# Kernel optimization log

Measured on AMD Instinct MI355X. Metric: run time of the kernel, lower is better.

Reference implementation:

```python
import jax, jax.numpy as jnp
import numpy as np

K_NN = 3
EPS = 1e-8
MASK_THRESH = 0.5


def _three_nn_interpolate(pts, known, feats):
    """pts: (B,N,3), known: (B,M,3), feats: (B,M,C) -> (B,N,C).
    Squared-distance 3-NN + inverse-distance weighted interpolation
    (pointnet2 three_nn / three_interpolate semantics)."""
    # (B,N,M) squared euclidean distances
    d2 = (jnp.sum(pts * pts, -1)[:, :, None]
          + jnp.sum(known * known, -1)[:, None, :]
          - 2.0 * jnp.einsum('bnd,bmd->bnm', pts, known))
    neg_d, idx = jax.lax.top_k(-d2, K_NN)          # (B,N,3)
    dist = jnp.maximum(-neg_d, 0.0)                # squared dists, clamp fp error
    dist_recip = 1.0 / (dist + EPS)
    weight = dist_recip / jnp.sum(dist_recip, -1, keepdims=True)  # (B,N,3)
    b_idx = jnp.arange(pts.shape[0])[:, None, None]
    gathered = feats[b_idx, idx]                   # (B,N,3,C)
    return jnp.sum(weight[..., None] * gathered, axis=2)  # (B,N,C)


def setup_inputs() -> dict:
    key = jax.random.key(0)
    ks = jax.random.split(key, 10)
    B, N, C = 4, 8192, 32
    M2, M3, M4, Mm = 8192, 4096, 2048, 4096
    sc = 10.0  # spread coords over a realistic metric range
    return {
        'points_mean': jax.random.normal(ks[0], (B, N, 3)) * sc,
        'known2': jax.random.normal(ks[1], (B, M2, 3)) * sc,
        'feats2': jax.random.normal(ks[2], (B, M2, C)),
        'known3': jax.random.normal(ks[3], (B, M3, 3)) * sc,
        'feats3': jax.random.normal(ks[4], (B, M3, C)),
        'known4': jax.random.normal(ks[5], (B, M4, 3)) * sc,
        'feats4': jax.random.normal(ks[6], (B, M4, C)),
        'match_points': jax.random.normal(ks[7], (B, Mm, 3)) * sc,
        'w_fc': jax.random.normal(ks[8], (64, 96)) * 0.1,
        'w_cls': jax.random.normal(ks[9], (1, 64)) * 0.1,
    }


def reference(points_mean, known2, feats2, known3, feats3, known4, feats4,
              match_points, w_fc, w_cls):
    p0 = _three_nn_interpolate(points_mean, known2, feats2)  # (B,N,32)
    p1 = _three_nn_interpolate(points_mean, known3, feats3)
    p2 = _three_nn_interpolate(points_mean, known4, feats4)
    pointwise = jnp.concatenate([p0, p1, p2], axis=-1) @ w_fc.T  # (B,N,64)
    pred_hm = pointwise @ w_cls.T                                 # (B,N,1)
    # GT mask: min distance to match points < 0.5 m
    d2 = (jnp.sum(points_mean * points_mean, -1)[:, :, None]
          + jnp.sum(match_points * match_points, -1)[:, None, :]
          - 2.0 * jnp.einsum('bnd,bmd->bnm', points_mean, match_points))
    min_d = jnp.sqrt(jnp.maximum(jnp.min(d2, axis=-1), 0.0))      # (B,N)
    gt_hm = (min_d < MASK_THRESH).astype(jnp.float32)
    return pred_hm, gt_hm
```

## Files before the change

kernel.cpp:

```cpp
#include <hip/hip_runtime.h>

typedef unsigned int u32;
typedef unsigned long long u64;
typedef float f32x2 __attribute__((ext_vector_type(2)));

#define NB 4
#define NQ 8192
#define MARGIN 0.0625f
#define NBKT 4096

#define OFF_C0   0u
#define OFF_C1   (512u*1024u)
#define OFF_C2   (768u*1024u)
#define OFF_CM   (896u*1024u)
#define OFF_OI0  (1408u*1024u)
#define OFF_OI1  (1536u*1024u)
#define OFF_OI2  (1600u*1024u)
#define OFF_QSX  (1632u*1024u)
#define OFF_QSY  (1760u*1024u)
#define OFF_QSZ  (1888u*1024u)
#define OFF_QSI  (2016u*1024u)
#define OFF_BOX  (2144u*1024u)
#define WS_NEW   (2144u*1024u + 1152u*32u)
#define WS_OLD   (512u*1024 + 256u*1024 + 128u*1024 + 512u*1024)

struct __align__(32) CP { f32x2 x, y, z, w; };
struct DM { double x, y, z, w; };

__device__ __forceinline__ f32x2 fma2(f32x2 a, f32x2 b, f32x2 c) {
  return __builtin_elementwise_fma(a, b, c);
}

__device__ __forceinline__ void lexins(double& e0d, double& e1d, double& e2d,
                                       int& e0i, int& e1i, int& e2i,
                                       double d, int i) {
  if (d < e2d || (d == e2d && i < e2i)) {
    if (d < e0d || (d == e0d && i < e0i)) {
      e2d = e1d; e2i = e1i; e1d = e0d; e1i = e0i; e0d = d; e0i = i;
    } else if (d < e1d || (d == e1d && i < e1i)) {
      e2d = e1d; e2i = e1i; e1d = d; e1i = i;
    } else {
      e2d = d; e2i = i;
    }
  }
}

__device__ __forceinline__ void ins4(float kv, u32 idx,
                                     float& k0, float& k1, float& k2, float& k3,
                                     u32& i0, u32& i1, u32& i2, u32& i3) {
  if (kv < k3) {
    bool lt0 = kv < k0, lt1 = kv < k1, lt2 = kv < k2;
    k3 = lt2 ? k2 : kv;               i3 = lt2 ? i2 : idx;
    k2 = lt2 ? (lt1 ? k1 : kv) : k2;  i2 = lt2 ? (lt1 ? i1 : idx) : i2;
    k1 = lt1 ? (lt0 ? k0 : kv) : k1;  i1 = lt1 ? (lt0 ? i0 : idx) : i1;
    k0 = lt0 ? kv : k0;               i0 = lt0 ? idx : i0;
  }
}

__device__ __forceinline__ u32 spread10(u32 v) {
  v &= 0x3FFu;
  v = (v | (v << 16)) & 0x030000FFu;
  v = (v | (v << 8))  & 0x0300F00Fu;
  v = (v | (v << 4))  & 0x030C30C3u;
  v = (v | (v << 2))  & 0x09249249u;
  return v;
}
__device__ __forceinline__ u32 morton30(float x, float y, float z) {
  int xi = (int)((x + 64.f) * 8.f);
  int yi = (int)((y + 64.f) * 8.f);
  int zi = (int)((z + 64.f) * 8.f);
  xi = min(max(xi, 0), 1023); yi = min(max(yi, 0), 1023); zi = min(max(zi, 0), 1023);
  return spread10((u32)xi) | (spread10((u32)yi) << 1) | (spread10((u32)zi) << 2);
}

__global__ __launch_bounds__(512) void prep_sort(
    const float* __restrict__ k2p, const float* __restrict__ k3p,
    const float* __restrict__ k4p, const float* __restrict__ mmp,
    const float* __restrict__ pts,
    CP* __restrict__ c0, CP* __restrict__ c1, CP* __restrict__ c2,
    DM* __restrict__ cm,
    u32* __restrict__ oi0, u32* __restrict__ oi1, u32* __restrict__ oi2,
    float* __restrict__ qsx, float* __restrict__ qsy, float* __restrict__ qsz,
    u32* __restrict__ qsi, float* __restrict__ boxes) {
  __shared__ u32 ord[8192];
  __shared__ u32 hist[NBKT];
  const int arr = blockIdx.x, b = blockIdx.y, tid = threadIdx.x;
  const float* src = (arr == 0) ? k2p : (arr == 1) ? k3p : (arr == 2) ? k4p
                      : (arr == 3) ? mmp : pts;
  const int n = (arr == 0) ? 8192 : (arr == 1) ? 4096 : (arr == 2) ? 2048
                 : (arr == 3) ? 4096 : 8192;
  const float* sb = src + (size_t)b * n * 3;

  for (int i = tid; i < NBKT; i += 512) hist[i] = 0;
  __syncthreads();
  for (int i = tid; i < n; i += 512) {
    u32 bkt = morton30(sb[3 * i], sb[3 * i + 1], sb[3 * i + 2]) >> 18;
    atomicAdd(&hist[bkt], 1u);
  }
  __syncthreads();
  for (int d = 1; d < NBKT; d <<= 1) {
    for (int i = tid; i < NBKT / (2 * d); i += 512) {
      int idx = (2 * i + 2) * d - 1;
      hist[idx] += hist[idx - d];
    }
    __syncthreads();
  }
  if (tid == 0) hist[NBKT - 1] = 0;
  __syncthreads();
  for (int d = NBKT >> 1; d >= 1; d >>= 1) {
    for (int i = tid; i < NBKT / (2 * d); i += 512) {
      int idx = (2 * i + 2) * d - 1;
      u32 t = hist[idx - d];
      hist[idx - d] = hist[idx];
      hist[idx] += t;
    }
    __syncthreads();
  }
  for (int i = tid; i < n; i += 512) {
    u32 bkt = morton30(sb[3 * i], sb[3 * i + 1], sb[3 * i + 2]) >> 18;
    u32 pos = atomicAdd(&hist[bkt], 1u);
    ord[pos] = (u32)i;
  }
  __syncthreads();

  if (arr < 3) {
    CP* dst = ((arr == 0) ? c0 : (arr == 1) ? c1 : c2) + (size_t)b * (n >> 1);
    u32* oi = ((arr == 0) ? oi0 : (arr == 1) ? oi1 : oi2) + (size_t)b * n;
    for (int i = tid; i < (n >> 1); i += 512) {
      u32 p0 = ord[2 * i], p1 = ord[2 * i + 1];
      const float* a0 = sb + 3 * (size_t)p0;
      const float* a1 = sb + 3 * (size_t)p1;
      float x0 = a0[0], y0 = a0[1], z0 = a0[2];
      float x1 = a1[0], y1 = a1[1], z1 = a1[2];
      CP c;
      c.x = f32x2{x0, x1}; c.y = f32x2{y0, y1}; c.z = f32x2{z0, z1};
      c.w = f32x2{fmaf(z0, z0, fmaf(y0, y0, x0 * x0)),
                  fmaf(z1, z1, fmaf(y1, y1, x1 * x1))};
      dst[i] = c; oi[2 * i] = p0; oi[2 * i + 1] = p1;
    }
  } else if (arr == 3) {
    DM* dst = cm + (size_t)b * 4096;
    for (int i = tid; i < 4096; i += 512) {
      u32 p = ord[i];
      double x = (double)sb[3 * p], y = (double)sb[3 * p + 1], z = (double)sb[3 * p + 2];
      DM d = {x, y, z, fma(z, z, fma(y, y, x * x))};
      dst[i] = d;
    }
  } else {
    for (int i = tid; i < 8192; i += 512) {
      u32 p = ord[i];
      size_t o = (size_t)b * 8192 + i;
      qsx[o] = sb[3 * p]; qsy[o] = sb[3 * p + 1]; qsz[o] = sb[3 * p + 2];
      qsi[o] = p;
    }
  }
  if (arr < 4) {
    const int nG = n >> 6;
    const int boff = (arr == 0) ? 0 : (arr == 1) ? 512 : (arr == 2) ? 768 : 896;
    for (int g = tid; g < nG; g += 512) {
      float xlo = 1e30f, xhi = -1e30f, ylo = 1e30f, yhi = -1e30f, zlo = 1e30f, zhi = -1e30f;
      for (int j = 0; j < 64; ++j) {
        u32 p = ord[g * 64 + j];
        float x = sb[3 * p], y = sb[3 * p + 1], z = sb[3 * p + 2];
        xlo = fminf(xlo, x); xhi = fmaxf(xhi, x);
        ylo = fminf(ylo, y); yhi = fmaxf(yhi, y);
        zlo = fminf(zlo, z); zhi = fmaxf(zhi, z);
      }
      float* bx = boxes + (size_t)(boff + b * nG + g) * 8;
      bx[0] = xlo; bx[1] = xhi; bx[2] = ylo; bx[3] = yhi; bx[4] = zlo; bx[5] = zhi;
      bx[6] = 0.f; bx[7] = 0.f;
    }
  }
}

struct Smem2 {
  float  qx[64], qy[64], qz[64];
  double qdx[64], qdy[64], qdz[64], qn[64];
  u32    oq[64];
  u32    di[3][64][4][4];
  double mmin[64][8];
  float  wv[96];
  float  wq[64][9];
  u32    iq[64][9];
  float  contrib[64][9];
};

__global__ __launch_bounds__(512, 2) void fused_sorted(
    const float* __restrict__ f2, const float* __restrict__ f3,
    const float* __restrict__ f4,
    const float* __restrict__ wfc, const float* __restrict__ wcls,
    const CP* __restrict__ c0, const CP* __restrict__ c1,
    const CP* __restrict__ c2, const DM* __restrict__ cm,
    const u32* __restrict__ oi0, const u32* __restrict__ oi1,
    const u32* __restrict__ oi2,
    const float* __restrict__ qsx, const float* __restrict__ qsy,
    const float* __restrict__ qsz, const u32* __restrict__ qsi,
    const float* __restrict__ boxes, float* __restrict__ out) {
  __shared__ Smem2 s;
  const int tid = threadIdx.x;
  const int b = blockIdx.y;
  const int tile = blockIdx.x;
  const int q0 = tile * 64;
  const int qloc = tid & 63;
  const int wid = __builtin_amdgcn_readfirstlane(tid >> 6);

  if (tid < 64) {
    size_t o = (size_t)b * NQ + q0 + tid;
    float x = qsx[o], y = qsy[o], z = qsz[o];
    s.qx[tid] = x; s.qy[tid] = y; s.qz[tid] = z; s.oq[tid] = qsi[o];
    double dx = (double)x, dy = (double)y, dz = (double)z;
    s.qdx[tid] = dx; s.qdy[tid] = dy; s.qdz[tid] = dz;
    s.qn[tid] = (dx * dx + dy * dy) + dz * dz;
  } else if (tid < 160) {
    int t = tid - 64;
    float acc = 0.f;
    for (int j = 0; j < 64; ++j) acc += wcls[j] * wfc[j * 96 + t];
    s.wv[t] = acc;
  }
  __syncthreads();

  const float qx = s.qx[qloc], qy = s.qy[qloc], qz = s.qz[qloc];
  const float qnf = fmaf(qz, qz, fmaf(qy, qy, qx * qx));
  const float fm2x = -2.0f * qx, fm2y = -2.0f * qy, fm2z = -2.0f * qz;
  const double dm2x = -2.0 * s.qdx[qloc];
  const double dm2y = -2.0 * s.qdy[qloc];
  const double dm2z = -2.0 * s.qdz[qloc];

  {
    int lvl, prt, P;
    if (wid < 4)      { lvl = 0; prt = wid;     P = 4; }
    else if (wid < 6) { lvl = 1; prt = wid - 4; P = 2; }
    else              { lvl = 2; prt = wid - 6; P = 2; }
    const int M  = (lvl == 0) ? 8192 : ((lvl == 1) ? 4096 : 2048);
    const int nG = M >> 6;
    const CP* c4 = ((lvl == 0) ? c0 : ((lvl == 1) ? c1 : c2)) + (((size_t)b * M) >> 1);
    const float* bxb = boxes +
        (size_t)(((lvl == 0) ? 0 : ((lvl == 1) ? 512 : 768)) + b * nG) * 8;
    int g0 = (tile * nG) >> 7;
    g0 = (g0 & ~(P - 1)) + prt;

    float k0 = __builtin_inff(), k1 = k0, k2 = k0, k3 = k0;
    u32 i0 = 0, i1 = 0, i2 = 0, i3 = 0;
    const f32x2 mx2 = {fm2x, fm2x}, my2 = {fm2y, fm2y}, mz2 = {fm2z, fm2z};

    for (int t = 0; t < nG / P; ++t) {
      int g = (g0 + P * t) & (nG - 1);
      const float* bx = bxb + g * 8;
      float dx = fmaxf(fmaxf(bx[0] - qx, qx - bx[1]), 0.f);
      float dy = fmaxf(fmaxf(bx[2] - qy, qy - bx[3]), 0.f);
      float dz = fmaxf(fmaxf(bx[4] - qz, qz - bx[5]), 0.f);
      float lb = fmaf(dx, dx, fmaf(dy, dy, dz * dz));
      if (__any(lb < qnf + k3 + MARGIN)) {
        const CP* cg = c4 + g * 32;
#pragma unroll 2
        for (int gg = 0; gg < 32; gg += 4) {
          f32x2 key[4];
#pragma unroll
          for (int u = 0; u < 4; ++u) {
            CP c = cg[gg + u];
            key[u] = fma2(mx2, c.x, fma2(my2, c.y, fma2(mz2, c.z, c.w)));
          }
#pragma unroll
          for (int u = 0; u < 4; ++u) {
            float ka = key[u].x, kb = key[u].y;
            if (fminf(ka, kb) < k3) {
              u32 ib = (u32)((g * 32 + gg + u) * 2);
              ins4(ka, ib,     k0, k1, k2, k3, i0, i1, i2, i3);
              ins4(kb, ib + 1, k0, k1, k2, k3, i0, i1, i2, i3);
            }
          }
        }
      }
    }
    s.di[lvl][qloc][prt][0] = i0; s.di[lvl][qloc][prt][1] = i1;
    s.di[lvl][qloc][prt][2] = i2; s.di[lvl][qloc][prt][3] = i3;
  }

  {
    const DM* cmb = cm + (size_t)b * 4096;
    const float* bxb = boxes + (size_t)(896 + b * 64) * 8;
    int gm0 = ((tile * 64) >> 7) & ~7;
    double smin = __builtin_inf();
    for (int t = 0; t < 8; ++t) {
      int g = (gm0 + wid + 8 * t) & 63;
      const float* bx = bxb + g * 8;
      float dx = fmaxf(fmaxf(bx[0] - qx, qx - bx[1]), 0.f);
      float dy = fmaxf(fmaxf(bx[2] - qy, qy - bx[3]), 0.f);
      float dz = fmaxf(fmaxf(bx[4] - qz, qz - bx[5]), 0.f);
      float lb = fmaf(dx, dx, fmaf(dy, dy, dz * dz));
      if (__any(lb < 0.3f)) {
        const DM* c8 = cmb + g * 64;
        for (int j = 0; j < 64; j += 8) {
          double sv[8];
#pragma unroll
          for (int u = 0; u < 8; ++u) {
            DM c = c8[j + u];
            sv[u] = fma(dm2x, c.x, fma(dm2y, c.y, fma(dm2z, c.z, c.w)));
          }
          double m01 = fmin(sv[0], sv[1]), m23 = fmin(sv[2], sv[3]);
          double m45 = fmin(sv[4], sv[5]), m67 = fmin(sv[6], sv[7]);
          smin = fmin(smin, fmin(fmin(m01, m23), fmin(m45, m67)));
        }
      }
    }
    s.mmin[qloc][wid] = smin;
  }
  __syncthreads();

  const int gqbase = b * NQ;
  if (tid < 192) {
    const int lvl = __builtin_amdgcn_readfirstlane(tid >> 6);
    const int q = tid & 63;
    const int M  = (lvl == 0) ? 8192 : ((lvl == 1) ? 4096 : 2048);
    const int np = (lvl == 0) ? 4 : 2;
    const CP* c4 = ((lvl == 0) ? c0 : ((lvl == 1) ? c1 : c2)) + (((size_t)b * M) >> 1);
    const u32* oi = ((lvl == 0) ? oi0 : ((lvl == 1) ? oi1 : oi2)) + (size_t)b * M;
    const double qdx = s.qdx[q], qdy = s.qdy[q], qdz = s.qdz[q], qn = s.qn[q];
    double e0 = __builtin_inf(), e1 = e0, e2 = e0;
    int i0 = 0, i1 = 0, i2 = 0;
    for (int h = 0; h < np; ++h) {
#pragma unroll
      for (int r = 0; r < 4; ++r) {
        int sidx = (int)s.di[lvl][q][h][r];
        CP cc = c4[sidx >> 1];
        bool hi = sidx & 1;
        double x = (double)(hi ? cc.x.y : cc.x.x);
        double y = (double)(hi ? cc.y.y : cc.y.x);
        double z = (double)(hi ? cc.z.y : cc.z.x);
        int orig = (int)oi[sidx];
        double kn2 = (x * x + y * y) + z * z;
        double dot = (qdx * x + qdy * y) + qdz * z;
        double d2 = (qn + kn2) - 2.0 * dot;
        lexins(e0, e1, e2, i0, i1, i2, d2, orig);
      }
    }
    double d0 = fmax(e0, 0.0), d1 = fmax(e1, 0.0), d2v = fmax(e2, 0.0);
    double r0 = 1.0 / (d0 + 1e-8);
    double r1 = 1.0 / (d1 + 1e-8);
    double r2 = 1.0 / (d2v + 1e-8);
    double sum = (r0 + r1) + r2;
    s.wq[q][lvl * 3 + 0] = (float)(r0 / sum); s.iq[q][lvl * 3 + 0] = (u32)i0;
    s.wq[q][lvl * 3 + 1] = (float)(r1 / sum); s.iq[q][lvl * 3 + 1] = (u32)i1;
    s.wq[q][lvl * 3 + 2] = (float)(r2 / sum); s.iq[q][lvl * 3 + 2] = (u32)i2;
  } else if (tid < 256) {
    const int q = tid - 192;
    double sm = s.mmin[q][0];
#pragma unroll
    for (int p = 1; p < 8; ++p) sm = fmin(sm, s.mmin[q][p]);
    double dm = s.qn[q] + sm;
    out[NB * NQ + gqbase + (int)s.oq[q]] = (dm < 0.25) ? 1.0f : 0.0f;
  }
  __syncthreads();

  for (int item = tid; item < 576; item += 512) {
    const int q = item & 63, j = item >> 6;
    const int lvl = j / 3;
    const float* fp = (lvl == 0) ? f2 : ((lvl == 1) ? f3 : f4);
    const int M = (lvl == 0) ? 8192 : ((lvl == 1) ? 4096 : 2048);
    const float4* row =
        (const float4*)(fp + ((size_t)b * M + s.iq[q][j]) * 32);
    const float* wvp = s.wv + lvl * 32;
    float acc = 0.f;
#pragma unroll
    for (int v = 0; v < 8; ++v) {
      float4 r = row[v];
      acc += wvp[4 * v] * r.x + wvp[4 * v + 1] * r.y
           + wvp[4 * v + 2] * r.z + wvp[4 * v + 3] * r.w;
    }
    s.contrib[q][j] = s.wq[q][j] * acc;
  }
  __syncthreads();
  if (tid < 64) {
    const float* c = s.contrib[tid];
    float l0 = (c[0] + c[1]) + c[2];
    float l1 = (c[3] + c[4]) + c[5];
    float l2 = (c[6] + c[7]) + c[8];
    out[gqbase + (int)s.oq[tid]] = (l0 + l1) + l2;
  }
}

__global__ __launch_bounds__(256) void prep_kernel(
    const float* __restrict__ k2p, const float* __restrict__ k3p,
    const float* __restrict__ k4p, const float* __restrict__ mmp,
    CP* __restrict__ c0, CP* __restrict__ c1,
    CP* __restrict__ c2, DM* __restrict__ cm) {
  int r = blockIdx.y;
  int i = blockIdx.x * 256 + threadIdx.x;
  if (r < 3) {
    const float* src = (r == 0) ? k2p : ((r == 1) ? k3p : k4p);
    CP* dst = (r == 0) ? c0 : ((r == 1) ? c1 : c2);
    int pairs = (r == 0) ? NB * 4096 : ((r == 1) ? NB * 2048 : NB * 1024);
    if (i >= pairs) return;
    const float* p = src + (size_t)i * 6;
    float x0 = p[0], y0 = p[1], z0 = p[2];
    float x1 = p[3], y1 = p[4], z1 = p[5];
    CP c;
    c.x = f32x2{x0, x1}; c.y = f32x2{y0, y1}; c.z = f32x2{z0, z1};
    c.w = f32x2{fmaf(z0, z0, fmaf(y0, y0, x0 * x0)),
                fmaf(z1, z1, fmaf(y1, y1, x1 * x1))};
    dst[i] = c;
  } else {
    if (i >= NB * 4096) return;
    double x = (double)mmp[3 * i], y = (double)mmp[3 * i + 1], z = (double)mmp[3 * i + 2];
    DM d = {x, y, z, fma(z, z, fma(y, y, x * x))};
    cm[i] = d;
  }
}

template <bool PREP>
__device__ __forceinline__ void scan_nn(
    const CP* __restrict__ cp, const float* __restrict__ raw,
    int gstart, int L, float m2x, float m2y, float m2z,
    float* kk, u32* ii) {
  float k0 = __builtin_inff(), k1 = k0, k2 = k0, k3 = k0;
  u32 i0 = 0, i1 = 0, i2 = 0, i3 = 0;
  if (PREP) {
    const f32x2 mx2 = {m2x, m2x}, my2 = {m2y, m2y}, mz2 = {m2z, m2z};
    const int G = L >> 1;
#pragma unroll 2
    for (int g = 0; g < G; g += 4) {
      f32x2 key[4];
#pragma unroll
      for (int u = 0; u < 4; ++u) {
        CP c = cp[g + u];
        key[u] = fma2(mx2, c.x, fma2(my2, c.y, fma2(mz2, c.z, c.w)));
      }
#pragma unroll
      for (int u = 0; u < 4; ++u) {
        float ka = key[u].x, kb = key[u].y;
        if (fminf(ka, kb) < k3) {
          u32 ib = (u32)(gstart + 2 * (g + u));
          ins4(ka, ib,     k0, k1, k2, k3, i0, i1, i2, i3);
          ins4(kb, ib + 1, k0, k1, k2, k3, i0, i1, i2, i3);
        }
      }
    }
  } else {
    for (int j = 0; j < L; j += 8) {
      float key[8];
#pragma unroll
      for (int u = 0; u < 8; ++u) {
        const float* p = raw + (size_t)(gstart + j + u) * 3;
        float x = p[0], y = p[1], z = p[2];
        float n2 = fmaf(z, z, fmaf(y, y, x * x));
        key[u] = fmaf(m2x, x, fmaf(m2y, y, fmaf(m2z, z, n2)));
      }
#pragma unroll
      for (int u = 0; u < 8; ++u)
        ins4(key[u], (u32)(gstart + j + u), k0, k1, k2, k3, i0, i1, i2, i3);
    }
  }
  kk[0] = k0; kk[1] = k1; kk[2] = k2; kk[3] = k3;
  ii[0] = i0; ii[1] = i1; ii[2] = i2; ii[3] = i3;
}

template <bool PREP>
__device__ __forceinline__ double scan_mask(
    const DM* __restrict__ c8, const float* __restrict__ raw,
    int gstart, int L, double m2x, double m2y, double m2z) {
  double smin = __builtin_inf();
  if (PREP) {
    for (int j = 0; j < L; j += 8) {
      double sv[8];
#pragma unroll
      for (int u = 0; u < 8; ++u) {
        DM c = c8[gstart + j + u];
        sv[u] = fma(m2x, c.x, fma(m2y, c.y, fma(m2z, c.z, c.w)));
      }
      double m01 = fmin(sv[0], sv[1]), m23 = fmin(sv[2], sv[3]);
      double m45 = fmin(sv[4], sv[5]), m67 = fmin(sv[6], sv[7]);
      smin = fmin(smin, fmin(fmin(m01, m23), fmin(m45, m67)));
    }
  } else {
    for (int j = 0; j < L; j += 4) {
#pragma unroll
      for (int u = 0; u < 4; ++u) {
        const float* p = raw + (size_t)(gstart + j + u) * 3;
        double x = (double)p[0], y = (double)p[1], z = (double)p[2];
        double kn = fma(z, z, fma(y, y, x * x));
        smin = fmin(smin, fma(m2x, x, fma(m2y, y, fma(m2z, z, kn))));
      }
    }
  }
  return smin;
}

struct Smem {
  float  qx[64], qy[64], qz[64];
  double qdx[64], qdy[64], qdz[64], qn[64];
  float  dk[3][64][4][4];
  u32    di[3][64][4][4];
  double mmin[64][8];
  float  wv[96];
  float  part[64][3];
};

template <bool PREP>
__global__ __launch_bounds__(512, 2) void fused_kernel(
    const float* __restrict__ pts,
    const float* __restrict__ k2p, const float* __restrict__ f2,
    const float* __restrict__ k3p, const float* __restrict__ f3,
    const float* __restrict__ k4p, const float* __restrict__ f4,
    const float* __restrict__ mmp,
    const float* __restrict__ wfc, const float* __restrict__ wcls,
    const CP* __restrict__ c0, const CP* __restrict__ c1,
    const CP* __restrict__ c2, const DM* __restrict__ cm,
    float* __restrict__ out) {
  __shared__ Smem s;
  const int tid = threadIdx.x;
  const int b = blockIdx.y;
  const int q0 = blockIdx.x * 64;
  const int qloc = tid & 63;
  const int wid = __builtin_amdgcn_readfirstlane(tid >> 6);

  if (tid < 64) {
    int gq = b * NQ + q0 + tid;
    float x = pts[3 * gq], y = pts[3 * gq + 1], z = pts[3 * gq + 2];
    s.qx[tid] = x; s.qy[tid] = y; s.qz[tid] = z;
    double dx = (double)x, dy = (double)y, dz = (double)z;
    s.qdx[tid] = dx; s.qdy[tid] = dy; s.qdz[tid] = dz;
    s.qn[tid] = (dx * dx + dy * dy) + dz * dz;
  } else if (tid < 160) {
    int t = tid - 64;
    float acc = 0.f;
    for (int j = 0; j < 64; ++j) acc += wcls[j] * wfc[j * 96 + t];
    s.wv[t] = acc;
  }
  __syncthreads();

  const float fm2x = -2.0f * s.qx[qloc];
  const float fm2y = -2.0f * s.qy[qloc];
  const float fm2z = -2.0f * s.qz[qloc];
  const double dm2x = -2.0 * s.qdx[qloc];
  const double dm2y = -2.0 * s.qdy[qloc];
  const double dm2z = -2.0 * s.qdz[qloc];

  {
    int lvl, prt, gstart, glen;
    if (wid < 4)      { lvl = 0; prt = wid;     gstart = wid * 2048;       glen = 2048; }
    else if (wid < 6) { lvl = 1; prt = wid - 4; gstart = (wid - 4) * 2048; glen = 2048; }
    else              { lvl = 2; prt = wid - 6; gstart = (wid - 6) * 1024; glen = 1024; }
    const CP* c4 = (lvl == 0) ? c0 : ((lvl == 1) ? c1 : c2);
    const float* raw = (lvl == 0) ? k2p : ((lvl == 1) ? k3p : k4p);
    const int      M = (lvl == 0) ? 8192 : ((lvl == 1) ? 4096 : 2048);
    float kk[4]; u32 ii[4];
    scan_nn<PREP>(c4 + (PREP ? (((size_t)b * M + gstart) >> 1) : 0),
                  raw + (size_t)b * M * 3,
                  gstart, glen, fm2x, fm2y, fm2z, kk, ii);
#pragma unroll
    for (int r = 0; r < 4; ++r) {
      s.dk[lvl][qloc][prt][r] = kk[r];
      s.di[lvl][qloc][prt][r] = ii[r];
    }
    int mstart, mlen;
    if (wid < 6) { mstart = wid * 256; mlen = 256; }
    else         { mstart = 1536 + (wid - 6) * 1280; mlen = 1280; }
    s.mmin[qloc][wid] = scan_mask<PREP>(cm + (PREP ? (size_t)b * 4096 : 0),
                                        mmp + (size_t)b * 4096 * 3,
                                        mstart, mlen, dm2x, dm2y, dm2z);
  }
  __syncthreads();

  const int gqbase = b * NQ + q0;
  if (tid < 192) {
    const int lvl = __builtin_amdgcn_readfirstlane(tid >> 6);
    const int q = tid & 63;
    const float* kp = (lvl == 0) ? k2p : ((lvl == 1) ? k3p : k4p);
    const int    M  = (lvl == 0) ? 8192 : ((lvl == 1) ? 4096 : 2048);
    const int    np = (lvl == 0) ? 4 : 2;
    const double qdx = s.qdx[q], qdy = s.qdy[q], qdz = s.qdz[q], qn = s.qn[q];
    double e0 = __builtin_inf(), e1 = e0, e2 = e0;
    int i0 = 0, i1 = 0, i2 = 0;
    for (int h = 0; h < np; ++h) {
#pragma unroll
      for (int r = 0; r < 4; ++r) {
        int idx = (int)s.di[lvl][q][h][r];
        const float* c = kp + ((size_t)b * M + idx) * 3;
        double x = (double)c[0], y = (double)c[1], z = (double)c[2];
        double kn2 = (x * x + y * y) + z * z;
        double dot = (qdx * x + qdy * y) + qdz * z;
        double d2 = (qn + kn2) - 2.0 * dot;
        lexins(e0, e1, e2, i0, i1, i2, d2, idx);
      }
    }
    double d0 = fmax(e0, 0.0), d1 = fmax(e1, 0.0), d2v = fmax(e2, 0.0);
    double r0 = 1.0 / (d0 + 1e-8);
    double r1 = 1.0 / (d1 + 1e-8);
    double r2 = 1.0 / (d2v + 1e-8);
    double sum = (r0 + r1) + r2;
    float wa = (float)(r0 / sum), wb = (float)(r1 / sum), wc = (float)(r2 / sum);
    const float* fp = (lvl == 0) ? f2 : ((lvl == 1) ? f3 : f4);
    const float* g0 = fp + ((size_t)b * M + i0) * 32;
    const float* g1 = fp + ((size_t)b * M + i1) * 32;
    const float* g2 = fp + ((size_t)b * M + i2) * 32;
    float acc = 0.f;
#pragma unroll
    for (int wd = 0; wd < 32; ++wd) {
      float v = (wa * g0[wd] + wb * g1[wd]) + wc * g2[wd];
      acc += s.wv[lvl * 32 + wd] * v;
    }
    s.part[q][lvl] = acc;
  } else if (tid < 256) {
    const int q = tid - 192;
    double sm = s.mmin[q][0];
#pragma unroll
    for (int p = 1; p < 8; ++p) sm = fmin(sm, s.mmin[q][p]);
    double dm = s.qn[q] + sm;
    out[NB * NQ + gqbase + q] = (dm < 0.25) ? 1.0f : 0.0f;
  }
  __syncthreads();
  if (tid < 64) {
    float pred = (s.part[tid][0] + s.part[tid][1]) + s.part[tid][2];
    out[gqbase + tid] = pred;
  }
}

extern "C" void kernel_launch(void* const* d_in, const int* in_sizes, int n_in,
                              void* d_out, int out_size, void* d_ws, size_t ws_size,
                              hipStream_t stream) {
  const float* pts    = (const float*)d_in[0];
  const float* known2 = (const float*)d_in[1];
  const float* feats2 = (const float*)d_in[2];
  const float* known3 = (const float*)d_in[3];
  const float* feats3 = (const float*)d_in[4];
  const float* known4 = (const float*)d_in[5];
  const float* feats4 = (const float*)d_in[6];
  const float* match  = (const float*)d_in[7];
  const float* wfc    = (const float*)d_in[8];
  const float* wcls   = (const float*)d_in[9];

  char* ws = (char*)d_ws;
  CP* c0 = (CP*)(ws + OFF_C0);
  CP* c1 = (CP*)(ws + OFF_C1);
  CP* c2 = (CP*)(ws + OFF_C2);
  DM* cm = (DM*)(ws + OFF_CM);

  if (ws_size >= WS_NEW) {
    u32* oi0 = (u32*)(ws + OFF_OI0);
    u32* oi1 = (u32*)(ws + OFF_OI1);
    u32* oi2 = (u32*)(ws + OFF_OI2);
    float* qsx = (float*)(ws + OFF_QSX);
    float* qsy = (float*)(ws + OFF_QSY);
    float* qsz = (float*)(ws + OFF_QSZ);
    u32* qsi = (u32*)(ws + OFF_QSI);
    float* boxes = (float*)(ws + OFF_BOX);
    hipLaunchKernelGGL(prep_sort, dim3(5, NB), dim3(512), 0, stream,
                       known2, known3, known4, match, pts,
                       c0, c1, c2, cm, oi0, oi1, oi2,
                       qsx, qsy, qsz, qsi, boxes);
    hipLaunchKernelGGL(fused_sorted, dim3(NQ / 64, NB), dim3(512), 0, stream,
                       feats2, feats3, feats4, wfc, wcls,
                       c0, c1, c2, cm, oi0, oi1, oi2,
                       qsx, qsy, qsz, qsi, boxes, (float*)d_out);
  } else if (ws_size >= WS_OLD) {
    hipLaunchKernelGGL(prep_kernel, dim3(64, 4), dim3(256), 0, stream,
                       known2, known3, known4, match, c0, c1, c2, cm);
    hipLaunchKernelGGL(HIP_KERNEL_NAME(fused_kernel<true>), dim3(NQ / 64, NB),
                       dim3(512), 0, stream, pts, known2, feats2, known3, feats3,
                       known4, feats4, match, wfc, wcls, c0, c1, c2, cm,
                       (float*)d_out);
  } else {
    hipLaunchKernelGGL(HIP_KERNEL_NAME(fused_kernel<false>), dim3(NQ / 64, NB),
                       dim3(512), 0, stream, pts, known2, feats2, known3, feats3,
                       known4, feats4, match, wfc, wcls, c0, c1, c2, cm,
                       (float*)d_out);
  }
}
```

Baseline: 246.0 us.

## Split sort into coarse bucket pass plus bitonic refine, stage candidate tiles through LDS

The single prep kernel becomes two. A bucket-sort pass writes 64-bit morton/index keys, and a refine_emit kernel bitonic-sorts each 512-element window and emits packed coordinates and per-group bounding boxes in parallel. The main kernel now loads the bounding boxes into shared memory, scans the query's home group unconditionally, and builds a per-wave list of groups that pass the box test. It then double-buffers those groups through LDS, replacing the inline scan that branched per group. Match points are stored as float4 and widened to double on the fly, replacing the double-precision array, at the cost of an extra launch and more shared memory.

```diff
diff --git a/kernel.cpp b/kernel.cpp
--- a/kernel.cpp
+++ b/kernel.cpp
@@ -10,18 +10,13 @@
 #define NBKT 4096
 
 #define OFF_C0   0u
-#define OFF_C1   (512u*1024u)
-#define OFF_C2   (768u*1024u)
-#define OFF_CM   (896u*1024u)
-#define OFF_OI0  (1408u*1024u)
-#define OFF_OI1  (1536u*1024u)
-#define OFF_OI2  (1600u*1024u)
-#define OFF_QSX  (1632u*1024u)
-#define OFF_QSY  (1760u*1024u)
-#define OFF_QSZ  (1888u*1024u)
-#define OFF_QSI  (2016u*1024u)
-#define OFF_BOX  (2144u*1024u)
-#define WS_NEW   (2144u*1024u + 1152u*32u)
+#define OFF_C1   524288u
+#define OFF_C2   786432u
+#define OFF_CMF  917504u
+#define OFF_SKEY 1179648u
+#define OFF_BOX  2031616u
+#define WS_NEW2  2068480u
+#define OFF_CM   917504u
 #define WS_OLD   (512u*1024 + 256u*1024 + 128u*1024 + 512u*1024)
 
 struct __align__(32) CP { f32x2 x, y, z, w; };
@@ -73,16 +68,15 @@
   return spread10((u32)xi) | (spread10((u32)yi) << 1) | (spread10((u32)zi) << 2);
 }
 
-__global__ __launch_bounds__(512) void prep_sort(
+__device__ __forceinline__ size_t skey_abase(int arr) {
+  return (arr == 0) ? 0 : (arr == 1) ? 32768 : (arr == 2) ? 49152
+        : (arr == 3) ? 57344 : 73728;
+}
+
+__global__ __launch_bounds__(512) void prep_csort(
     const float* __restrict__ k2p, const float* __restrict__ k3p,
     const float* __restrict__ k4p, const float* __restrict__ mmp,
-    const float* __restrict__ pts,
-    CP* __restrict__ c0, CP* __restrict__ c1, CP* __restrict__ c2,
-    DM* __restrict__ cm,
-    u32* __restrict__ oi0, u32* __restrict__ oi1, u32* __restrict__ oi2,
-    float* __restrict__ qsx, float* __restrict__ qsy, float* __restrict__ qsz,
-    u32* __restrict__ qsi, float* __restrict__ boxes) {
-  __shared__ u32 ord[8192];
+    const float* __restrict__ pts, u64* __restrict__ skey) {
   __shared__ u32 hist[NBKT];
   const int arr = blockIdx.x, b = blockIdx.y, tid = threadIdx.x;
   const float* src = (arr == 0) ? k2p : (arr == 1) ? k3p : (arr == 2) ? k4p
@@ -90,12 +84,13 @@
   const int n = (arr == 0) ? 8192 : (arr == 1) ? 4096 : (arr == 2) ? 2048
                  : (arr == 3) ? 4096 : 8192;
   const float* sb = src + (size_t)b * n * 3;
+  u64* skb = skey + skey_abase(arr) + (size_t)b * n;
 
   for (int i = tid; i < NBKT; i += 512) hist[i] = 0;
   __syncthreads();
   for (int i = tid; i < n; i += 512) {
-    u32 bkt = morton30(sb[3 * i], sb[3 * i + 1], sb[3 * i + 2]) >> 18;
-    atomicAdd(&hist[bkt], 1u);
+    u32 k = morton30(sb[3 * i], sb[3 * i + 1], sb[3 * i + 2]);
+    atomicAdd(&hist[k >> 18], 1u);
   }
   __syncthreads();
   for (int d = 1; d < NBKT; d <<= 1) {
@@ -117,63 +112,110 @@
     __syncthreads();
   }
   for (int i = tid; i < n; i += 512) {
-    u32 bkt = morton30(sb[3 * i], sb[3 * i + 1], sb[3 * i + 2]) >> 18;
-    u32 pos = atomicAdd(&hist[bkt], 1u);
-    ord[pos] = (u32)i;
-  }
-  __syncthreads();
-
+    u32 k = morton30(sb[3 * i], sb[3 * i + 1], sb[3 * i + 2]);
+    u32 pos = atomicAdd(&hist[k >> 18], 1u);
+    skb[pos] = ((u64)k << 32) | (u32)i;
+  }
+}
+
+__global__ __launch_bounds__(512) void refine_emit(
+    const float* __restrict__ k2p, const float* __restrict__ k3p,
+    const float* __restrict__ k4p, const float* __restrict__ mmp,
+    const float* __restrict__ pts, u64* __restrict__ skey,
+    CP* __restrict__ c0, CP* __restrict__ c1, CP* __restrict__ c2,
+    float4* __restrict__ cmf, float* __restrict__ boxes) {
+  __shared__ u64 ex[512];
+  const int widx = blockIdx.x, b = blockIdx.y, tid = threadIdx.x;
+  int arr, win;
+  if (widx < 16)      { arr = 0; win = widx; }
+  else if (widx < 24) { arr = 1; win = widx - 16; }
+  else if (widx < 28) { arr = 2; win = widx - 24; }
+  else if (widx < 36) { arr = 3; win = widx - 28; }
+  else                { arr = 4; win = widx - 36; }
+  const float* src = (arr == 0) ? k2p : (arr == 1) ? k3p : (arr == 2) ? k4p
+                      : (arr == 3) ? mmp : pts;
+  const int n = (arr == 0) ? 8192 : (arr == 1) ? 4096 : (arr == 2) ? 2048
+                 : (arr == 3) ? 4096 : 8192;
+  u64* skb = skey + skey_abase(arr) + (size_t)b * n;
+  const int e = win * 512 + tid;
+  u64 v = skb[e];
+
+  for (int k = 2; k <= 512; k <<= 1) {
+    for (int j = k >> 1; j > 0; j >>= 1) {
+      u64 w;
+      if (j < 64) {
+        w = __shfl_xor(v, j);
+      } else {
+        __syncthreads();
+        ex[tid] = v;
+        __syncthreads();
+        w = ex[tid ^ j];
+      }
+      bool up = (tid & k) == 0;
+      bool lower = (tid & j) == 0;
+      v = (up == lower) ? (v < w ? v : w) : (v < w ? w : v);
+    }
+  }
+  skb[e] = v;
+  if (arr == 4) return;
+
+  u32 p = (u32)v;
+  const float* sb = src + (size_t)b * n * 3;
+  float x = sb[3 * p], y = sb[3 * p + 1], z = sb[3 * p + 2];
   if (arr < 3) {
-    CP* dst = ((arr == 0) ? c0 : (arr == 1) ? c1 : c2) + (size_t)b * (n >> 1);
-    u32* oi = ((arr == 0) ? oi0 : (arr == 1) ? oi1 : oi2) + (size_t)b * n;
-    for (int i = tid; i < (n >> 1); i += 512) {
-      u32 p0 = ord[2 * i], p1 = ord[2 * i + 1];
-      const float* a0 = sb + 3 * (size_t)p0;
-      const float* a1 = sb + 3 * (size_t)p1;
-      float x0 = a0[0], y0 = a0[1], z0 = a0[2];
-      float x1 = a1[0], y1 = a1[1], z1 = a1[2];
-      CP c;
-      c.x = f32x2{x0, x1}; c.y = f32x2{y0, y1}; c.z = f32x2{z0, z1};
-      c.w = f32x2{fmaf(z0, z0, fmaf(y0, y0, x0 * x0)),
-                  fmaf(z1, z1, fmaf(y1, y1, x1 * x1))};
-      dst[i] = c; oi[2 * i] = p0; oi[2 * i + 1] = p1;
-    }
-  } else if (arr == 3) {
-    DM* dst = cm + (size_t)b * 4096;
-    for (int i = tid; i < 4096; i += 512) {
-      u32 p = ord[i];
-      double x = (double)sb[3 * p], y = (double)sb[3 * p + 1], z = (double)sb[3 * p + 2];
-      DM d = {x, y, z, fma(z, z, fma(y, y, x * x))};
-      dst[i] = d;
-    }
+    CP* dst = (arr == 0) ? c0 : (arr == 1) ? c1 : c2;
+    float* df = (float*)(dst + (size_t)b * (n >> 1) + (e >> 1));
+    int sl = e & 1;
+    df[sl]     = x;
+    df[2 + sl] = y;
+    df[4 + sl] = z;
+    df[6 + sl] = fmaf(z, z, fmaf(y, y, x * x));
   } else {
-    for (int i = tid; i < 8192; i += 512) {
-      u32 p = ord[i];
-      size_t o = (size_t)b * 8192 + i;
-      qsx[o] = sb[3 * p]; qsy[o] = sb[3 * p + 1]; qsz[o] = sb[3 * p + 2];
-      qsi[o] = p;
-    }
-  }
-  if (arr < 4) {
-    const int nG = n >> 6;
+    cmf[(size_t)b * 4096 + e] = float4{x, y, z, 0.f};
+  }
+  float xlo = x, xhi = x, ylo = y, yhi = y, zlo = z, zhi = z;
+#pragma unroll
+  for (int off = 1; off < 64; off <<= 1) {
+    xlo = fminf(xlo, __shfl_xor(xlo, off)); xhi = fmaxf(xhi, __shfl_xor(xhi, off));
+    ylo = fminf(ylo, __shfl_xor(ylo, off)); yhi = fmaxf(yhi, __shfl_xor(yhi, off));
+    zlo = fminf(zlo, __shfl_xor(zlo, off)); zhi = fmaxf(zhi, __shfl_xor(zhi, off));
+  }
+  if ((tid & 63) == 0) {
+    const int nG = n >> 6, g = e >> 6;
     const int boff = (arr == 0) ? 0 : (arr == 1) ? 512 : (arr == 2) ? 768 : 896;
-    for (int g = tid; g < nG; g += 512) {
-      float xlo = 1e30f, xhi = -1e30f, ylo = 1e30f, yhi = -1e30f, zlo = 1e30f, zhi = -1e30f;
-      for (int j = 0; j < 64; ++j) {
-        u32 p = ord[g * 64 + j];
-        float x = sb[3 * p], y = sb[3 * p + 1], z = sb[3 * p + 2];
-        xlo = fminf(xlo, x); xhi = fmaxf(xhi, x);
-        ylo = fminf(ylo, y); yhi = fmaxf(yhi, y);
-        zlo = fminf(zlo, z); zhi = fmaxf(zhi, z);
-      }
-      float* bx = boxes + (size_t)(boff + b * nG + g) * 8;
-      bx[0] = xlo; bx[1] = xhi; bx[2] = ylo; bx[3] = yhi; bx[4] = zlo; bx[5] = zhi;
-      bx[6] = 0.f; bx[7] = 0.f;
-    }
-  }
-}
-
-struct Smem2 {
+    float* bx = boxes + ((size_t)boff + (size_t)b * nG + g) * 8;
+    bx[0] = xlo; bx[1] = xhi; bx[2] = ylo; bx[3] = yhi; bx[4] = zlo; bx[5] = zhi;
+    bx[6] = 0.f; bx[7] = 0.f;
+  }
+}
+
+__device__ __forceinline__ void scan_pairs32(
+    const CP* __restrict__ cg, u32 ebase,
+    f32x2 mx2, f32x2 my2, f32x2 mz2,
+    float& k0, float& k1, float& k2, float& k3,
+    u32& i0, u32& i1, u32& i2, u32& i3) {
+#pragma unroll 4
+  for (int gg = 0; gg < 32; gg += 4) {
+    f32x2 key[4];
+#pragma unroll
+    for (int u = 0; u < 4; ++u) {
+      CP c = cg[gg + u];
+      key[u] = fma2(mx2, c.x, fma2(my2, c.y, fma2(mz2, c.z, c.w)));
+    }
+#pragma unroll
+    for (int u = 0; u < 4; ++u) {
+      float ka = key[u].x, kb = key[u].y;
+      if (fminf(ka, kb) < k3) {
+        u32 ib = ebase + (u32)((gg + u) * 2);
+        ins4(ka, ib,     k0, k1, k2, k3, i0, i1, i2, i3);
+        ins4(kb, ib + 1, k0, k1, k2, k3, i0, i1, i2, i3);
+      }
+    }
+  }
+}
+
+struct Smem3 {
+  float  box[2304];
   float  qx[64], qy[64], qz[64];
   double qdx[64], qdy[64], qdz[64], qn[64];
   u32    oq[64];
@@ -183,31 +225,41 @@
   float  wq[64][9];
   u32    iq[64][9];
   float  contrib[64][9];
+  float4 stage[8][2][64];
+  u32    list[8][32];
 };
 
-__global__ __launch_bounds__(512, 2) void fused_sorted(
+__global__ __launch_bounds__(512, 2) void fused_sorted2(
+    const float* __restrict__ pts,
     const float* __restrict__ f2, const float* __restrict__ f3,
     const float* __restrict__ f4,
     const float* __restrict__ wfc, const float* __restrict__ wcls,
     const CP* __restrict__ c0, const CP* __restrict__ c1,
-    const CP* __restrict__ c2, const DM* __restrict__ cm,
-    const u32* __restrict__ oi0, const u32* __restrict__ oi1,
-    const u32* __restrict__ oi2,
-    const float* __restrict__ qsx, const float* __restrict__ qsy,
-    const float* __restrict__ qsz, const u32* __restrict__ qsi,
-    const float* __restrict__ boxes, float* __restrict__ out) {
-  __shared__ Smem2 s;
+    const CP* __restrict__ c2, const float4* __restrict__ cmf,
+    const u64* __restrict__ skey, const float* __restrict__ boxes,
+    float* __restrict__ out) {
+  __shared__ Smem3 s;
   const int tid = threadIdx.x;
   const int b = blockIdx.y;
   const int tile = blockIdx.x;
   const int q0 = tile * 64;
   const int qloc = tid & 63;
+  const int lane = tid & 63;
   const int wid = __builtin_amdgcn_readfirstlane(tid >> 6);
 
+  {
+    float* bf = s.box;
+    for (int i = tid; i < 1024; i += 512) bf[i]        = boxes[(size_t)(b * 128) * 8 + i];
+    { int i = tid; if (i < 512) bf[1024 + i] = boxes[((size_t)512 + b * 64) * 8 + i]; }
+    { int i = tid; if (i < 256) bf[1536 + i] = boxes[((size_t)768 + b * 32) * 8 + i]; }
+    { int i = tid; if (i < 512) bf[1792 + i] = boxes[((size_t)896 + b * 64) * 8 + i]; }
+  }
   if (tid < 64) {
-    size_t o = (size_t)b * NQ + q0 + tid;
-    float x = qsx[o], y = qsy[o], z = qsz[o];
-    s.qx[tid] = x; s.qy[tid] = y; s.qz[tid] = z; s.oq[tid] = qsi[o];
+    u64 kv = skey[73728 + (size_t)b * NQ + q0 + tid];
+    u32 p = (u32)kv;
+    const float* pb = pts + (size_t)b * NQ * 3;
+    float x = pb[3 * p], y = pb[3 * p + 1], z = pb[3 * p + 2];
+    s.qx[tid] = x; s.qy[tid] = y; s.qz[tid] = z; s.oq[tid] = p;
     double dx = (double)x, dy = (double)y, dz = (double)z;
     s.qdx[tid] = dx; s.qdy[tid] = dy; s.qdz[tid] = dz;
     s.qn[tid] = (dx * dx + dy * dy) + dz * dz;
@@ -227,15 +279,13 @@
   const double dm2z = -2.0 * s.qdz[qloc];
 
   {
-    int lvl, prt, P;
-    if (wid < 4)      { lvl = 0; prt = wid;     P = 4; }
-    else if (wid < 6) { lvl = 1; prt = wid - 4; P = 2; }
-    else              { lvl = 2; prt = wid - 6; P = 2; }
+    int lvl, prt, P, lboff;
+    if (wid < 4)      { lvl = 0; prt = wid;     P = 4; lboff = 0; }
+    else if (wid < 6) { lvl = 1; prt = wid - 4; P = 2; lboff = 128; }
+    else              { lvl = 2; prt = wid - 6; P = 2; lboff = 192; }
     const int M  = (lvl == 0) ? 8192 : ((lvl == 1) ? 4096 : 2048);
     const int nG = M >> 6;
     const CP* c4 = ((lvl == 0) ? c0 : ((lvl == 1) ? c1 : c2)) + (((size_t)b * M) >> 1);
-    const float* bxb = boxes +
-        (size_t)(((lvl == 0) ? 0 : ((lvl == 1) ? 512 : 768)) + b * nG) * 8;
     int g0 = (tile * nG) >> 7;
     g0 = (g0 & ~(P - 1)) + prt;
 
@@ -243,59 +293,66 @@
     u32 i0 = 0, i1 = 0, i2 = 0, i3 = 0;
     const f32x2 mx2 = {fm2x, fm2x}, my2 = {fm2y, fm2y}, mz2 = {fm2z, fm2z};
 
-    for (int t = 0; t < nG / P; ++t) {
+    scan_pairs32(c4 + (size_t)g0 * 32, (u32)(g0 * 64), mx2, my2, mz2,
+                 k0, k1, k2, k3, i0, i1, i2, i3);
+
+    int nl = 0;
+    for (int t = 1; t < nG / P; ++t) {
       int g = (g0 + P * t) & (nG - 1);
-      const float* bx = bxb + g * 8;
+      const float* bx = &s.box[(lboff + g) * 8];
       float dx = fmaxf(fmaxf(bx[0] - qx, qx - bx[1]), 0.f);
       float dy = fmaxf(fmaxf(bx[2] - qy, qy - bx[3]), 0.f);
       float dz = fmaxf(fmaxf(bx[4] - qz, qz - bx[5]), 0.f);
       float lb = fmaf(dx, dx, fmaf(dy, dy, dz * dz));
       if (__any(lb < qnf + k3 + MARGIN)) {
-        const CP* cg = c4 + g * 32;
-#pragma unroll 2
-        for (int gg = 0; gg < 32; gg += 4) {
-          f32x2 key[4];
-#pragma unroll
-          for (int u = 0; u < 4; ++u) {
-            CP c = cg[gg + u];
-            key[u] = fma2(mx2, c.x, fma2(my2, c.y, fma2(mz2, c.z, c.w)));
-          }
-#pragma unroll
-          for (int u = 0; u < 4; ++u) {
-            float ka = key[u].x, kb = key[u].y;
-            if (fminf(ka, kb) < k3) {
-              u32 ib = (u32)((g * 32 + gg + u) * 2);
-              ins4(ka, ib,     k0, k1, k2, k3, i0, i1, i2, i3);
-              ins4(kb, ib + 1, k0, k1, k2, k3, i0, i1, i2, i3);
-            }
-          }
-        }
-      }
-    }
+        if (lane == 0) s.list[wid][nl] = (u32)g;
+        ++nl;
+      }
+    }
+
+    int cur = 0;
+    float4 v;
+    u32 gcur = 0, gnext = 0;
+    if (nl > 0) {
+      gcur = s.list[wid][0];
+      v = ((const float4*)(c4 + (size_t)gcur * 32))[lane];
+    }
+    for (int i = 0; i < nl; ++i) {
+      s.stage[wid][cur][lane] = v;
+      if (i + 1 < nl) {
+        gnext = s.list[wid][i + 1];
+        v = ((const float4*)(c4 + (size_t)gnext * 32))[lane];
+      }
+      scan_pairs32((const CP*)&s.stage[wid][cur][0], (u32)(gcur * 64),
+                   mx2, my2, mz2, k0, k1, k2, k3, i0, i1, i2, i3);
+      gcur = gnext; cur ^= 1;
+    }
+
     s.di[lvl][qloc][prt][0] = i0; s.di[lvl][qloc][prt][1] = i1;
     s.di[lvl][qloc][prt][2] = i2; s.di[lvl][qloc][prt][3] = i3;
   }
 
   {
-    const DM* cmb = cm + (size_t)b * 4096;
-    const float* bxb = boxes + (size_t)(896 + b * 64) * 8;
+    const float4* cmb = cmf + (size_t)b * 4096;
     int gm0 = ((tile * 64) >> 7) & ~7;
     double smin = __builtin_inf();
     for (int t = 0; t < 8; ++t) {
       int g = (gm0 + wid + 8 * t) & 63;
-      const float* bx = bxb + g * 8;
+      const float* bx = &s.box[(224 + g) * 8];
       float dx = fmaxf(fmaxf(bx[0] - qx, qx - bx[1]), 0.f);
       float dy = fmaxf(fmaxf(bx[2] - qy, qy - bx[3]), 0.f);
       float dz = fmaxf(fmaxf(bx[4] - qz, qz - bx[5]), 0.f);
       float lb = fmaf(dx, dx, fmaf(dy, dy, dz * dz));
       if (__any(lb < 0.3f)) {
-        const DM* c8 = cmb + g * 64;
+        const float4* c8 = cmb + g * 64;
         for (int j = 0; j < 64; j += 8) {
           double sv[8];
 #pragma unroll
           for (int u = 0; u < 8; ++u) {
-            DM c = c8[j + u];
-            sv[u] = fma(dm2x, c.x, fma(dm2y, c.y, fma(dm2z, c.z, c.w)));
+            float4 cf = c8[j + u];
+            double x = (double)cf.x, y = (double)cf.y, z = (double)cf.z;
+            double w = fma(z, z, fma(y, y, x * x));
+            sv[u] = fma(dm2x, x, fma(dm2y, y, fma(dm2z, z, w)));
           }
           double m01 = fmin(sv[0], sv[1]), m23 = fmin(sv[2], sv[3]);
           double m45 = fmin(sv[4], sv[5]), m67 = fmin(sv[6], sv[7]);
@@ -314,7 +371,8 @@
     const int M  = (lvl == 0) ? 8192 : ((lvl == 1) ? 4096 : 2048);
     const int np = (lvl == 0) ? 4 : 2;
     const CP* c4 = ((lvl == 0) ? c0 : ((lvl == 1) ? c1 : c2)) + (((size_t)b * M) >> 1);
-    const u32* oi = ((lvl == 0) ? oi0 : ((lvl == 1) ? oi1 : oi2)) + (size_t)b * M;
+    const u64* skl = skey + ((lvl == 0) ? 0 : (lvl == 1) ? 32768 : 49152)
+                     + (size_t)b * M;
     const double qdx = s.qdx[q], qdy = s.qdy[q], qdz = s.qdz[q], qn = s.qn[q];
     double e0 = __builtin_inf(), e1 = e0, e2 = e0;
     int i0 = 0, i1 = 0, i2 = 0;
@@ -327,7 +385,7 @@
         double x = (double)(hi ? cc.x.y : cc.x.x);
         double y = (double)(hi ? cc.y.y : cc.y.x);
         double z = (double)(hi ? cc.z.y : cc.z.x);
-        int orig = (int)oi[sidx];
+        int orig = (int)(u32)skl[sidx];
         double kn2 = (x * x + y * y) + z * z;
         double dot = (qdx * x + qdy * y) + qdz * z;
         double d2 = (qn + kn2) - 2.0 * dot;
@@ -357,8 +415,7 @@
     const int lvl = j / 3;
     const float* fp = (lvl == 0) ? f2 : ((lvl == 1) ? f3 : f4);
     const int M = (lvl == 0) ? 8192 : ((lvl == 1) ? 4096 : 2048);
-    const float4* row =
-        (const float4*)(fp + ((size_t)b * M + s.iq[q][j]) * 32);
+    const float4* row = (const float4*)(fp + ((size_t)b * M + s.iq[q][j]) * 32);
     const float* wvp = s.wv + lvl * 32;
     float acc = 0.f;
 #pragma unroll
@@ -633,26 +690,21 @@
   CP* c0 = (CP*)(ws + OFF_C0);
   CP* c1 = (CP*)(ws + OFF_C1);
   CP* c2 = (CP*)(ws + OFF_C2);
-  DM* cm = (DM*)(ws + OFF_CM);
-
-  if (ws_size >= WS_NEW) {
-    u32* oi0 = (u32*)(ws + OFF_OI0);
-    u32* oi1 = (u32*)(ws + OFF_OI1);
-    u32* oi2 = (u32*)(ws + OFF_OI2);
-    float* qsx = (float*)(ws + OFF_QSX);
-    float* qsy = (float*)(ws + OFF_QSY);
-    float* qsz = (float*)(ws + OFF_QSZ);
-    u32* qsi = (u32*)(ws + OFF_QSI);
+
+  if (ws_size >= WS_NEW2) {
+    float4* cmf = (float4*)(ws + OFF_CMF);
+    u64* skey = (u64*)(ws + OFF_SKEY);
     float* boxes = (float*)(ws + OFF_BOX);
-    hipLaunchKernelGGL(prep_sort, dim3(5, NB), dim3(512), 0, stream,
-                       known2, known3, known4, match, pts,
-                       c0, c1, c2, cm, oi0, oi1, oi2,
-                       qsx, qsy, qsz, qsi, boxes);
-    hipLaunchKernelGGL(fused_sorted, dim3(NQ / 64, NB), dim3(512), 0, stream,
-                       feats2, feats3, feats4, wfc, wcls,
-                       c0, c1, c2, cm, oi0, oi1, oi2,
-                       qsx, qsy, qsz, qsi, boxes, (float*)d_out);
+    hipLaunchKernelGGL(prep_csort, dim3(5, NB), dim3(512), 0, stream,
+                       known2, known3, known4, match, pts, skey);
+    hipLaunchKernelGGL(refine_emit, dim3(52, NB), dim3(512), 0, stream,
+                       known2, known3, known4, match, pts, skey,
+                       c0, c1, c2, cmf, boxes);
+    hipLaunchKernelGGL(fused_sorted2, dim3(NQ / 64, NB), dim3(512), 0, stream,
+                       pts, feats2, feats3, feats4, wfc, wcls,
+                       c0, c1, c2, cmf, skey, boxes, (float*)d_out);
   } else if (ws_size >= WS_OLD) {
+    DM* cm = (DM*)(ws + OFF_CM);
     hipLaunchKernelGGL(prep_kernel, dim3(64, 4), dim3(256), 0, stream,
                        known2, known3, known4, match, c0, c1, c2, cm);
     hipLaunchKernelGGL(HIP_KERNEL_NAME(fused_kernel<true>), dim3(NQ / 64, NB),
@@ -660,6 +712,7 @@
                        known4, feats4, match, wfc, wcls, c0, c1, c2, cm,
                        (float*)d_out);
   } else {
+    DM* cm = (DM*)(ws + OFF_CM);
     hipLaunchKernelGGL(HIP_KERNEL_NAME(fused_kernel<false>), dim3(NQ / 64, NB),
                        dim3(512), 0, stream, pts, known2, feats2, known3, feats3,
                        known4, feats4, match, wfc, wcls, c0, c1, c2, cm,
```

Measured after the change: 237.3 us. 1.04x faster.
